# Performance work log

Measured on AMD Instinct MI355X. Metric: run time of the kernel, lower is better.

The kernel has to match this reference:

```python
import jax, jax.numpy as jnp
import numpy as np

D_MODEL = 1024
N_HEADS = 16
D_K = D_MODEL // N_HEADS


def setup_inputs() -> dict:
    key = jax.random.key(0)
    ks = jax.random.split(key, 7)
    B, S, D = 2, 2048, D_MODEL
    scale = 1.0 / np.sqrt(D)
    return {
        "query": jax.random.normal(ks[0], (B, S, D), dtype=jnp.float32),
        "key": jax.random.normal(ks[1], (B, S, D), dtype=jnp.float32),
        "value": jax.random.normal(ks[2], (B, S, D), dtype=jnp.float32),
        "w_q": jax.random.normal(ks[3], (D, D), dtype=jnp.float32) * scale,
        "w_k": jax.random.normal(ks[4], (D, D), dtype=jnp.float32) * scale,
        "w_v": jax.random.normal(ks[5], (D, D), dtype=jnp.float32) * scale,
        "w_o": jax.random.normal(ks[6], (D, D), dtype=jnp.float32) * scale,
    }


def reference(query, key, value, w_q, w_k, w_v, w_o):
    B, S, D = query.shape
    H, Dk = N_HEADS, D_K
    # nn.Linear (no bias): x @ W.T ; then split heads -> [B, H, S, Dk]
    def split_heads(x, W):
        return (x @ W.T).reshape(B, S, H, Dk).transpose(0, 2, 1, 3)
    Q = split_heads(query, w_q)
    K = split_heads(key, w_k)
    V = split_heads(value, w_v)
    scores = jnp.einsum("bhqd,bhkd->bhqk", Q, K) / np.sqrt(Dk).astype(jnp.float32)
    attn = jax.nn.softmax(scores, axis=-1)  # dropout is identity in eval
    attended = jnp.einsum("bhqk,bhkd->bhqd", attn, V)
    attended = attended.transpose(0, 2, 1, 3).reshape(B, S, D)
    output = attended @ w_o.T
    avg_attention = attn.mean(axis=1)  # mean over heads -> [B, S, S]
    return (output, avg_attention)
```

## Files before the change

### kernel.cpp

```cpp
#include <hip/hip_runtime.h>
#include <math.h>

#define SEQ 2048
#define DMODEL 1024
#define NH 16
#define DK 64
#define BATCH 2

using bf16x8 = __attribute__((ext_vector_type(8))) __bf16;
using bf16x4 = __attribute__((ext_vector_type(4))) __bf16;
using f32x4  = __attribute__((ext_vector_type(4))) float;

__device__ inline f32x4 mfma16(bf16x8 a, bf16x8 b, f32x4 c) {
    return __builtin_amdgcn_mfma_f32_16x16x32_bf16(a, b, c, 0, 0, 0);
}

__device__ inline void load_lds16(const void* g, void* l) {
    __builtin_amdgcn_global_load_lds(
        (const __attribute__((address_space(1))) void*)g,
        (__attribute__((address_space(3))) void*)l, 16, 0, 0);
}

#define BARRIER() __builtin_amdgcn_s_barrier()
#define EXP_SCALE 0.18033688011112042f
#define EXP2(x) __builtin_amdgcn_exp2f(x)

__global__ __launch_bounds__(256) void conv_bf16(
        const float* __restrict__ q, const float* __restrict__ k,
        const float* __restrict__ v, const float* __restrict__ wq,
        const float* __restrict__ wk, const float* __restrict__ wv,
        const float* __restrict__ wo,
        __bf16* __restrict__ oq, __bf16* __restrict__ ok, __bf16* __restrict__ ov,
        __bf16* __restrict__ owq, __bf16* __restrict__ owk,
        __bf16* __restrict__ owv, __bf16* __restrict__ owo) {
    int bid = blockIdx.x;
    const float* src;
    __bf16* dst;
    size_t off;
    if (bid < 3072) {
        int ti = bid >> 10;
        src = ti == 0 ? q : (ti == 1 ? k : v);
        dst = ti == 0 ? oq : (ti == 1 ? ok : ov);
        off = (size_t)(bid & 1023) * 4096;
    } else {
        int ti = (bid - 3072) >> 8;
        src = ti == 0 ? wq : (ti == 1 ? wk : (ti == 2 ? wv : wo));
        dst = ti == 0 ? owq : (ti == 1 ? owk : (ti == 2 ? owv : owo));
        off = (size_t)((bid - 3072) & 255) * 4096;
    }
    src += off; dst += off;
    const int t = threadIdx.x;
#pragma unroll
    for (int i = 0; i < 4; ++i) {
        float4 x = *(const float4*)(src + t * 4 + i * 1024);
        bf16x4 y;
        y[0] = (__bf16)x.x; y[1] = (__bf16)x.y;
        y[2] = (__bf16)x.z; y[3] = (__bf16)x.w;
        *(bf16x4*)(dst + t * 4 + i * 1024) = y;
    }
}

__device__ __forceinline__ void gemm_core(const __bf16* __restrict__ A,
                                          const __bf16* __restrict__ B,
                                          void* __restrict__ out, int mode,
                                          int m0, int n0, int N,
                                          __bf16* As, __bf16* Bs) {
    const int t    = threadIdx.x;
    const int w    = t >> 6;
    const int lane = t & 63;
    const int m    = lane & 15;
    const int kg   = lane >> 4;
    const int wr   = w >> 1, wc = w & 1;

    f32x4 acc[4][2] = {};

    for (int k0 = 0; k0 < 1024; k0 += 64) {
        __syncthreads();
#pragma unroll
        for (int i = 0; i < 4; ++i) {
            const int ablk = w * 4 + i;
            const int mt = ablk >> 1, kt = ablk & 1;
            const __bf16* ga = A + (size_t)(m0 + mt * 16 + m) * 1024 + k0 + kt * 32 + kg * 8;
            load_lds16(ga, &As[ablk * 512]);
        }
#pragma unroll
        for (int i = 0; i < 2; ++i) {
            const int bblk = w * 2 + i;
            const int nt = bblk >> 1, kt = bblk & 1;
            const __bf16* gb = B + (size_t)(n0 + nt * 16 + m) * 1024 + k0 + kt * 32 + kg * 8;
            load_lds16(gb, &Bs[bblk * 512]);
        }
        __syncthreads();
#pragma unroll
        for (int kt = 0; kt < 2; ++kt) {
            bf16x8 af[4], bg[2];
#pragma unroll
            for (int i = 0; i < 4; ++i)
                af[i] = *(const bf16x8*)&As[((wr * 4 + i) * 2 + kt) * 512 + lane * 8];
#pragma unroll
            for (int j = 0; j < 2; ++j)
                bg[j] = *(const bf16x8*)&Bs[((wc * 2 + j) * 2 + kt) * 512 + lane * 8];
#pragma unroll
            for (int i = 0; i < 4; ++i)
#pragma unroll
                for (int j = 0; j < 2; ++j)
                    acc[i][j] = mfma16(af[i], bg[j], acc[i][j]);
        }
    }

#pragma unroll
    for (int i = 0; i < 4; ++i) {
        const int rb = m0 + wr * 64 + i * 16 + kg * 4;
#pragma unroll
        for (int j = 0; j < 2; ++j) {
            const int gc = n0 + wc * 32 + j * 16 + m;
#pragma unroll
            for (int r = 0; r < 4; ++r) {
                const int gr = rb + r;
                const float vv = acc[i][j][r];
                if (mode == 0) {
                    ((float*)out)[(size_t)gr * N + gc] = vv;
                } else if (mode == 1) {
                    ((__bf16*)out)[(size_t)gr * N + gc] = (__bf16)vv;
                } else {
                    const int hh = gr >> 6, dd = gr & 63;
                    const int bb = gc >> 11, ss = gc & 2047;
                    ((__bf16*)out)[(((size_t)bb * NH + hh) * DK + dd) * SEQ + ss] = (__bf16)vv;
                }
            }
        }
    }
}

__device__ __forceinline__ int xcd_swz(int s, int cpx) {
    return (s & 7) * cpx + (s >> 3);
}

__global__ __launch_bounds__(256) void gemm_qkv(
        const __bf16* __restrict__ Xq, const __bf16* __restrict__ Wq, __bf16* Qr,
        const __bf16* __restrict__ Xk, const __bf16* __restrict__ Wk, __bf16* Kr,
        const __bf16* __restrict__ Xv, const __bf16* __restrict__ Wv, __bf16* Vt) {
    __shared__ __align__(16) __bf16 As[8192];
    __shared__ __align__(16) __bf16 Bs[4096];
    const int bid = blockIdx.x;
    if (bid < 512) {
        const int s = xcd_swz(bid, 64);
        gemm_core(Xq, Wq, Qr, 1, (s >> 4) * 128, (s & 15) * 64, 1024, As, Bs);
    } else if (bid < 1024) {
        const int s = xcd_swz(bid - 512, 64);
        gemm_core(Xk, Wk, Kr, 1, (s >> 4) * 128, (s & 15) * 64, 1024, As, Bs);
    } else {
        const int s = xcd_swz(bid - 1024, 64);
        gemm_core(Wv, Xv, Vt, 2, (s >> 6) * 128, (s & 63) * 64, 4096, As, Bs);
    }
}

__global__ __launch_bounds__(512, 4) void attn_flash(const __bf16* __restrict__ Qr,
                                                     const __bf16* __restrict__ Kr,
                                                     const __bf16* __restrict__ Vt,
                                                     __bf16* __restrict__ att,
                                                     float* __restrict__ invs) {
    __shared__ __align__(16) unsigned char smem[66048];
    __bf16* Ks   = (__bf16*)smem;
    __bf16* Vs   = (__bf16*)(smem + 16384);
    __bf16* Pb   = (__bf16*)(smem + 32768);
    float*  sinv = (float*)(smem + 65536);

    const int t    = threadIdx.x;
    const int w    = t >> 6;
    const int lane = t & 63;
    const int m    = lane & 15;
    const int kg   = lane >> 4;

    const int L  = xcd_swz(blockIdx.x, 64);
    const int b  = L >> 8;
    const int h  = (L >> 4) & 15;
    const int qw = (L & 15) * 128 + w * 16;

    const __bf16* Kh = Kr + (size_t)b * SEQ * 1024 + h * 64;
    const __bf16* Vh = Vt + ((size_t)b * NH + h) * DK * SEQ;
    __bf16* Pw = Pb + w * 2048;

    const size_t rowQ = (size_t)(b * SEQ + qw + m) * 1024 + h * 64 + kg * 8;
    const bf16x8 qa = *(const bf16x8*)(Qr + rowQ);
    const bf16x8 qb = *(const bf16x8*)(Qr + rowQ + 32);

    const int rk0 = t >> 3,          ck0 = t & 7;
    const int rk1 = (t + 512) >> 3,  ck1 = (t + 512) & 7;
    const int rv0 = t >> 4,          cv0 = t & 15;
    const int rv1 = (t + 512) >> 4,  cv1 = (t + 512) & 15;
    bf16x8 kst0, kst1, vst0, vst1;

    auto issue = [&](int kt) {
        kst0 = *(const bf16x8*)(Kh + (size_t)(kt + rk0) * 1024 + ck0 * 8);
        kst1 = *(const bf16x8*)(Kh + (size_t)(kt + rk1) * 1024 + ck1 * 8);
        vst0 = *(const bf16x8*)(Vh + (size_t)rv0 * SEQ + kt + cv0 * 8);
        vst1 = *(const bf16x8*)(Vh + (size_t)rv1 * SEQ + kt + cv1 * 8);
    };
    auto commit = [&]() {
        *(bf16x8*)&Ks[rk0 * 64 + ((ck0 ^ (rk0 & 7)) * 8)] = kst0;
        *(bf16x8*)&Ks[rk1 * 64 + ((ck1 ^ (rk1 & 7)) * 8)] = kst1;
        *(bf16x8*)&Vs[rv0 * 128 + ((cv0 ^ (rv0 & 7)) * 8)] = vst0;
        *(bf16x8*)&Vs[rv1 * 128 + ((cv1 ^ (rv1 & 7)) * 8)] = vst1;
    };

    f32x4 pv[4] = {};
    float rsum = 0.f;

    issue(0);
    commit();
    __syncthreads();

    for (int kt = 0; kt < SEQ; kt += 128) {
        if (kt + 128 < SEQ) issue(kt + 128);
#pragma unroll
        for (int nt = 0; nt < 8; ++nt) {
            const int row = nt * 16 + m;
            bf16x8 k0 = *(const bf16x8*)&Ks[row * 64 + ((kg ^ (m & 7)) * 8)];
            bf16x8 k1 = *(const bf16x8*)&Ks[row * 64 + (((kg + 4) ^ (m & 7)) * 8)];
            f32x4 c = {};
            c = mfma16(k0, qa, c);
            c = mfma16(k1, qb, c);
            bf16x4 pk;
#pragma unroll
            for (int r = 0; r < 4; ++r) {
                float p = EXP2(c[r] * EXP_SCALE);
                rsum += p;
                pk[r] = (__bf16)p;
            }
            const int up = (nt * 2 + (kg >> 1)) ^ (m & 7);
            *(bf16x4*)&Pw[m * 128 + (((up << 1) | (kg & 1)) * 4)] = pk;
        }
#pragma unroll
        for (int ks = 0; ks < 4; ++ks) {
            const int u = (ks * 4 + kg) ^ (m & 7);
            bf16x8 pa = *(const bf16x8*)&Pw[m * 128 + u * 8];
#pragma unroll
            for (int nt = 0; nt < 4; ++nt) {
                const int rv = nt * 16 + m;
                bf16x8 vb = *(const bf16x8*)&Vs[rv * 128 + u * 8];
                pv[nt] = mfma16(pa, vb, pv[nt]);
            }
        }
        __syncthreads();
        if (kt + 128 < SEQ) {
            commit();
            asm volatile("s_waitcnt lgkmcnt(0)" ::: "memory");
            BARRIER();
        }
    }

    rsum += __shfl_xor(rsum, 16);
    rsum += __shfl_xor(rsum, 32);
    const float inv = 1.0f / rsum;
    if (lane < 16) {
        sinv[w * 16 + m] = inv;
        invs[((size_t)b * NH + h) * SEQ + qw + m] = inv;
    }
    __syncthreads();
    float iv[4];
#pragma unroll
    for (int r = 0; r < 4; ++r) iv[r] = sinv[w * 16 + kg * 4 + r];

    float* scf = (float*)smem + w * 1088;
#pragma unroll
    for (int nt = 0; nt < 4; ++nt)
#pragma unroll
        for (int r = 0; r < 4; ++r)
            scf[(kg * 4 + r) * 68 + nt * 16 + m] = pv[nt][r] * iv[r];
    __syncthreads();
    {
        const int q = lane >> 2, c0 = (lane & 3) * 16;
        const float* srcf = &scf[q * 68 + c0];
        bf16x8 o0, o1;
#pragma unroll
        for (int j = 0; j < 8; ++j) {
            o0[j] = (__bf16)srcf[j];
            o1[j] = (__bf16)srcf[j + 8];
        }
        __bf16* dst = att + (size_t)(b * SEQ + qw + q) * DMODEL + h * DK + c0;
        *(bf16x8*)(dst)     = o0;
        *(bf16x8*)(dst + 8) = o1;
    }
}

__device__ __forceinline__ void avg_core(const __bf16* __restrict__ Qr,
                                         const __bf16* __restrict__ Kr,
                                         const float* __restrict__ invs,
                                         float* __restrict__ avg,
                                         int L, __bf16* Kb) {
    const int t    = threadIdx.x;
    const int w    = t >> 6;
    const int lane = t & 63;
    const int m    = lane & 15;
    const int kg   = lane >> 4;
    const int b    = L >> 9;
    const int s0   = ((L >> 5) & 15) * 128;
    const int qw   = (L & 31) * 64 + w * 16;

    const __bf16* Kbase = Kr + (size_t)(b * SEQ + s0) * 1024;

    auto stageK = [&](int buf, int h) {
#pragma unroll
        for (int s = 0; s < 4; ++s) {
            const int i   = w * 4 + s;
            const int row = i * 8 + (lane >> 3);
            const int u   = lane & 7;
            load_lds16(Kbase + (size_t)row * 1024 + h * 64 + ((u ^ (row & 7)) * 8),
                       Kb + buf * 8192 + i * 512);
        }
    };

    f32x4 acc[8] = {};

    stageK(0, 0);
    const size_t qoff = (size_t)(b * SEQ + qw + m) * 1024 + kg * 8;
    bf16x8 a0 = *(const bf16x8*)(Qr + qoff);
    bf16x8 a1 = *(const bf16x8*)(Qr + qoff + 32);
    f32x4 ivr = *(const f32x4*)&invs[(size_t)b * NH * SEQ + qw + kg * 4];
    __syncthreads();

    int cur = 0;
    for (int h = 0; h < NH; ++h) {
        if (h + 1 < NH) stageK(cur ^ 1, h + 1);
        bf16x8 na0, na1;
        f32x4 nivr;
        if (h + 1 < NH) {
            na0  = *(const bf16x8*)(Qr + qoff + (h + 1) * 64);
            na1  = *(const bf16x8*)(Qr + qoff + (h + 1) * 64 + 32);
            nivr = *(const f32x4*)&invs[((size_t)b * NH + h + 1) * SEQ + qw + kg * 4];
        }
        const __bf16* Kc = Kb + cur * 8192;
#pragma unroll
        for (int nt = 0; nt < 8; ++nt) {
            const int row = nt * 16 + m;
            bf16x8 k0 = *(const bf16x8*)&Kc[row * 64 + ((kg ^ (m & 7)) * 8)];
            bf16x8 k1 = *(const bf16x8*)&Kc[row * 64 + (((kg + 4) ^ (m & 7)) * 8)];
            f32x4 c = {};
            c = mfma16(a0, k0, c);
            c = mfma16(a1, k1, c);
#pragma unroll
            for (int r = 0; r < 4; ++r)
                acc[nt][r] += ivr[r] * EXP2(c[r] * EXP_SCALE);
        }
        __syncthreads();
        cur ^= 1;
        a0 = na0; a1 = na1; ivr = nivr;
    }

    const float sc = 1.0f / NH;
#pragma unroll
    for (int nt = 0; nt < 8; ++nt)
#pragma unroll
        for (int r = 0; r < 4; ++r)
            avg[(size_t)(b * SEQ + qw + kg * 4 + r) * SEQ + s0 + nt * 16 + m] =
                acc[nt][r] * sc;
}

__global__ __launch_bounds__(256) void gemm_wo_avg(
        const __bf16* __restrict__ At, const __bf16* __restrict__ Wo,
        float* __restrict__ out,
        const __bf16* __restrict__ Qr, const __bf16* __restrict__ Kr,
        const float* __restrict__ invs, float* __restrict__ avg) {
    __shared__ __align__(16) __bf16 sm[16384];
    const int bid = blockIdx.x;
    if (bid < 512) {
        const int s = xcd_swz(bid, 64);
        gemm_core(At, Wo, out, 0, (s >> 4) * 128, (s & 15) * 64, 1024,
                  sm, sm + 8192);
    } else {
        avg_core(Qr, Kr, invs, avg, xcd_swz(bid - 512, 128), sm);
    }
}

extern "C" void kernel_launch(void* const* d_in, const int* in_sizes, int n_in,
                              void* d_out, int out_size, void* d_ws, size_t ws_size,
                              hipStream_t stream) {
    const float* query = (const float*)d_in[0];
    const float* key   = (const float*)d_in[1];
    const float* value = (const float*)d_in[2];
    const float* w_q   = (const float*)d_in[3];
    const float* w_k   = (const float*)d_in[4];
    const float* w_v   = (const float*)d_in[5];
    const float* w_o   = (const float*)d_in[6];

    float* out = (float*)d_out;
    float* avg = out + (size_t)BATCH * SEQ * DMODEL;

    __bf16* Xq = (__bf16*)d_ws;
    __bf16* Xk = Xq + 4194304;
    __bf16* Xv = Xk + 4194304;
    __bf16* Wq = Xv + 4194304;
    __bf16* Wk = Wq + 1048576;
    __bf16* Wv = Wk + 1048576;
    __bf16* Wo = Wv + 1048576;
    __bf16* Qr = Wo + 1048576;
    __bf16* Kr = Qr + 4194304;
    __bf16* Vt = Kr + 4194304;
    float*  Invs = (float*)(Vt + 4194304);
    __bf16* At = Xq;

    conv_bf16<<<4096, 256, 0, stream>>>(query, key, value, w_q, w_k, w_v, w_o,
                                        Xq, Xk, Xv, Wq, Wk, Wv, Wo);

    gemm_qkv<<<1536, 256, 0, stream>>>(Xq, Wq, Qr, Xk, Wk, Kr, Xv, Wv, Vt);

    attn_flash<<<512, 512, 0, stream>>>(Qr, Kr, Vt, At, Invs);

    gemm_wo_avg<<<1536, 256, 0, stream>>>(At, Wo, out, Qr, Kr, Invs, avg);
}
```

Baseline: 292.2 us.

## Triple-buffer GEMM core with async LDS loads and 128x128 tiles

Rewrites the shared GEMM core to use a three-stage ring of LDS buffers filled by global_load_lds, with explicit vmcnt waits so loads for future K-steps overlap the MFMA work on the current one. The K-step shrinks to 32 and the output tile grows from 128x64 to 128x128, so each wave runs 16 MFMAs per step and reuses its fragments more. Wave priority is raised around the MFMA block. Grids for the QKV and output-projection GEMMs are halved to match, and launch bounds request 3 blocks per CU. The cost is more LDS per block, more accumulator registers, and fewer blocks in flight.

```diff
diff --git a/kernel.cpp b/kernel.cpp
--- a/kernel.cpp
+++ b/kernel.cpp
@@ -21,7 +21,9 @@
         (__attribute__((address_space(3))) void*)l, 16, 0, 0);
 }
 
+#define VMCNT(n) asm volatile("s_waitcnt vmcnt(" #n ")" ::: "memory")
 #define BARRIER() __builtin_amdgcn_s_barrier()
+#define CFENCE() asm volatile("" ::: "memory")
 #define EXP_SCALE 0.18033688011112042f
 #define EXP2(x) __builtin_amdgcn_exp2f(x)
 
@@ -72,48 +74,62 @@
     const int kg   = lane >> 4;
     const int wr   = w >> 1, wc = w & 1;
 
-    f32x4 acc[4][2] = {};
-
-    for (int k0 = 0; k0 < 1024; k0 += 64) {
-        __syncthreads();
-#pragma unroll
-        for (int i = 0; i < 4; ++i) {
-            const int ablk = w * 4 + i;
-            const int mt = ablk >> 1, kt = ablk & 1;
-            const __bf16* ga = A + (size_t)(m0 + mt * 16 + m) * 1024 + k0 + kt * 32 + kg * 8;
-            load_lds16(ga, &As[ablk * 512]);
-        }
-#pragma unroll
-        for (int i = 0; i < 2; ++i) {
-            const int bblk = w * 2 + i;
-            const int nt = bblk >> 1, kt = bblk & 1;
-            const __bf16* gb = B + (size_t)(n0 + nt * 16 + m) * 1024 + k0 + kt * 32 + kg * 8;
-            load_lds16(gb, &Bs[bblk * 512]);
-        }
-        __syncthreads();
-#pragma unroll
-        for (int kt = 0; kt < 2; ++kt) {
-            bf16x8 af[4], bg[2];
-#pragma unroll
-            for (int i = 0; i < 4; ++i)
-                af[i] = *(const bf16x8*)&As[((wr * 4 + i) * 2 + kt) * 512 + lane * 8];
-#pragma unroll
-            for (int j = 0; j < 2; ++j)
-                bg[j] = *(const bf16x8*)&Bs[((wc * 2 + j) * 2 + kt) * 512 + lane * 8];
-#pragma unroll
-            for (int i = 0; i < 4; ++i)
-#pragma unroll
-                for (int j = 0; j < 2; ++j)
-                    acc[i][j] = mfma16(af[i], bg[j], acc[i][j]);
-        }
+    auto stage = [&](int buf, int k0) {
+        const __bf16* ga0 = A + (size_t)(m0 + w * 16 + m) * 1024 + k0 + kg * 8;
+        load_lds16(ga0, &As[buf * 4096 + w * 512]);
+        const __bf16* ga1 = A + (size_t)(m0 + (w + 4) * 16 + m) * 1024 + k0 + kg * 8;
+        load_lds16(ga1, &As[buf * 4096 + (w + 4) * 512]);
+        const __bf16* gb0 = B + (size_t)(n0 + w * 16 + m) * 1024 + k0 + kg * 8;
+        load_lds16(gb0, &Bs[buf * 4096 + w * 512]);
+        const __bf16* gb1 = B + (size_t)(n0 + (w + 4) * 16 + m) * 1024 + k0 + kg * 8;
+        load_lds16(gb1, &Bs[buf * 4096 + (w + 4) * 512]);
+    };
+
+    f32x4 acc[4][4] = {};
+
+    stage(0, 0);
+    CFENCE();
+    stage(1, 32);
+
+    int cb = 0, sb = 2;
+    for (int ts = 0; ts < 32; ++ts) {
+        if (ts < 30) {
+            stage(sb, (ts + 2) * 32);
+            VMCNT(8);
+        } else if (ts == 30) {
+            VMCNT(4);
+        } else {
+            VMCNT(0);
+        }
+        BARRIER();
+        CFENCE();
+        const __bf16* Ac = &As[cb * 4096];
+        const __bf16* Bc = &Bs[cb * 4096];
+        bf16x8 af[4], bg[4];
+#pragma unroll
+        for (int i = 0; i < 4; ++i)
+            af[i] = *(const bf16x8*)&Ac[(wr * 4 + i) * 512 + lane * 8];
+#pragma unroll
+        for (int j = 0; j < 4; ++j)
+            bg[j] = *(const bf16x8*)&Bc[(wc * 4 + j) * 512 + lane * 8];
+        __builtin_amdgcn_s_setprio(1);
+#pragma unroll
+        for (int i = 0; i < 4; ++i)
+#pragma unroll
+            for (int j = 0; j < 4; ++j)
+                acc[i][j] = mfma16(af[i], bg[j], acc[i][j]);
+        __builtin_amdgcn_s_setprio(0);
+        BARRIER();
+        cb = cb == 2 ? 0 : cb + 1;
+        sb = sb == 2 ? 0 : sb + 1;
     }
 
 #pragma unroll
     for (int i = 0; i < 4; ++i) {
         const int rb = m0 + wr * 64 + i * 16 + kg * 4;
 #pragma unroll
-        for (int j = 0; j < 2; ++j) {
-            const int gc = n0 + wc * 32 + j * 16 + m;
+        for (int j = 0; j < 4; ++j) {
+            const int gc = n0 + wc * 64 + j * 16 + m;
 #pragma unroll
             for (int r = 0; r < 4; ++r) {
                 const int gr = rb + r;
@@ -136,22 +152,22 @@
     return (s & 7) * cpx + (s >> 3);
 }
 
-__global__ __launch_bounds__(256) void gemm_qkv(
+__global__ __launch_bounds__(256, 3) void gemm_qkv(
         const __bf16* __restrict__ Xq, const __bf16* __restrict__ Wq, __bf16* Qr,
         const __bf16* __restrict__ Xk, const __bf16* __restrict__ Wk, __bf16* Kr,
         const __bf16* __restrict__ Xv, const __bf16* __restrict__ Wv, __bf16* Vt) {
-    __shared__ __align__(16) __bf16 As[8192];
-    __shared__ __align__(16) __bf16 Bs[4096];
+    __shared__ __align__(16) __bf16 As[12288];
+    __shared__ __align__(16) __bf16 Bs[12288];
     const int bid = blockIdx.x;
-    if (bid < 512) {
-        const int s = xcd_swz(bid, 64);
-        gemm_core(Xq, Wq, Qr, 1, (s >> 4) * 128, (s & 15) * 64, 1024, As, Bs);
-    } else if (bid < 1024) {
-        const int s = xcd_swz(bid - 512, 64);
-        gemm_core(Xk, Wk, Kr, 1, (s >> 4) * 128, (s & 15) * 64, 1024, As, Bs);
+    if (bid < 256) {
+        const int s = xcd_swz(bid, 32);
+        gemm_core(Xq, Wq, Qr, 1, (s >> 3) * 128, (s & 7) * 128, 1024, As, Bs);
+    } else if (bid < 512) {
+        const int s = xcd_swz(bid - 256, 32);
+        gemm_core(Xk, Wk, Kr, 1, (s >> 3) * 128, (s & 7) * 128, 1024, As, Bs);
     } else {
-        const int s = xcd_swz(bid - 1024, 64);
-        gemm_core(Wv, Xv, Vt, 2, (s >> 6) * 128, (s & 63) * 64, 4096, As, Bs);
+        const int s = xcd_swz(bid - 512, 32);
+        gemm_core(Wv, Xv, Vt, 2, (s >> 5) * 128, (s & 31) * 128, 4096, As, Bs);
     }
 }
 
@@ -357,19 +373,19 @@
                 acc[nt][r] * sc;
 }
 
-__global__ __launch_bounds__(256) void gemm_wo_avg(
+__global__ __launch_bounds__(256, 3) void gemm_wo_avg(
         const __bf16* __restrict__ At, const __bf16* __restrict__ Wo,
         float* __restrict__ out,
         const __bf16* __restrict__ Qr, const __bf16* __restrict__ Kr,
         const float* __restrict__ invs, float* __restrict__ avg) {
-    __shared__ __align__(16) __bf16 sm[16384];
+    __shared__ __align__(16) __bf16 sm[24576];
     const int bid = blockIdx.x;
-    if (bid < 512) {
-        const int s = xcd_swz(bid, 64);
-        gemm_core(At, Wo, out, 0, (s >> 4) * 128, (s & 15) * 64, 1024,
-                  sm, sm + 8192);
+    if (bid < 256) {
+        const int s = xcd_swz(bid, 32);
+        gemm_core(At, Wo, out, 0, (s >> 3) * 128, (s & 7) * 128, 1024,
+                  sm, sm + 12288);
     } else {
-        avg_core(Qr, Kr, invs, avg, xcd_swz(bid - 512, 128), sm);
+        avg_core(Qr, Kr, invs, avg, xcd_swz(bid - 256, 128), sm);
     }
 }
 
@@ -403,9 +419,9 @@
     conv_bf16<<<4096, 256, 0, stream>>>(query, key, value, w_q, w_k, w_v, w_o,
                                         Xq, Xk, Xv, Wq, Wk, Wv, Wo);
 
-    gemm_qkv<<<1536, 256, 0, stream>>>(Xq, Wq, Qr, Xk, Wk, Kr, Xv, Wv, Vt);
+    gemm_qkv<<<768, 256, 0, stream>>>(Xq, Wq, Qr, Xk, Wk, Kr, Xv, Wv, Vt);
 
     attn_flash<<<512, 512, 0, stream>>>(Qr, Kr, Vt, At, Invs);
 
-    gemm_wo_avg<<<1536, 256, 0, stream>>>(At, Wo, out, Qr, Kr, Invs, avg);
-}
+    gemm_wo_avg<<<1280, 256, 0, stream>>>(At, Wo, out, Qr, Kr, Invs, avg);
+}
```

New measurement: 263.6 us. 1.11x faster.
